# Optimization experiments

Measured on AMD Instinct MI355X. Metric: run time of the kernel, lower is better.

The kernel has to match this reference:

```python
import jax, jax.numpy as jnp
import numpy as np

D_MODEL, N_HEAD, N_KV_HEAD, D_HEAD = 1024, 16, 4, 64


def rotate_half(x):
    x1, x2 = x[..., : x.shape[-1] // 2], x[..., x.shape[-1] // 2:]
    return jnp.concatenate((-x2, x1), axis=-1)


def rope_cos_sin(seq_len, dim, dtype=jnp.float32):
    inv_freq = 1.0 / (10000.0 ** (jnp.arange(0, dim, 2, dtype=jnp.float32) / dim))
    t = jnp.arange(seq_len, dtype=jnp.float32)
    freqs = jnp.einsum('i,j->ij', t, inv_freq)          # [S, dim/2]
    emb = jnp.concatenate((freqs, freqs), axis=-1)       # [S, dim]
    return jnp.cos(emb).astype(dtype), jnp.sin(emb).astype(dtype)


def setup_inputs() -> dict:
    key = jax.random.key(0)
    ks = jax.random.split(key, 5)
    B, S = 2, 2048
    scale = 0.02
    return {
        'x': jax.random.normal(ks[0], (B, S, D_MODEL), dtype=jnp.float32),
        'Wq': jax.random.normal(ks[1], (D_MODEL, N_HEAD * D_HEAD), dtype=jnp.float32) * scale,
        'Wk': jax.random.normal(ks[2], (D_MODEL, N_KV_HEAD * D_HEAD), dtype=jnp.float32) * scale,
        'Wv': jax.random.normal(ks[3], (D_MODEL, N_KV_HEAD * D_HEAD), dtype=jnp.float32) * scale,
        'Wo': jax.random.normal(ks[4], (N_HEAD * D_HEAD, D_MODEL), dtype=jnp.float32) * scale,
    }


def reference(x, Wq, Wk, Wv, Wo):
    B, S, _ = x.shape
    scale = 1.0 / np.sqrt(D_HEAD)
    # projections -> [B, H, S, Dh]
    q = (x @ Wq).reshape(B, S, N_HEAD, D_HEAD).transpose(0, 2, 1, 3)
    k = (x @ Wk).reshape(B, S, N_KV_HEAD, D_HEAD).transpose(0, 2, 1, 3)
    v = (x @ Wv).reshape(B, S, N_KV_HEAD, D_HEAD).transpose(0, 2, 1, 3)
    cos, sin = rope_cos_sin(S, D_HEAD, x.dtype)          # [S, Dh]
    q = q * cos + rotate_half(q) * sin
    k = k * cos + rotate_half(k) * sin
    rep = N_HEAD // N_KV_HEAD
    k = jnp.repeat(k, rep, axis=1)                       # [B, H, S, Dh]
    v = jnp.repeat(v, rep, axis=1)
    scores = jnp.einsum('bhqd,bhkd->bhqk', q, k) * scale # [B, H, S, S]
    causal = jnp.triu(jnp.ones((S, S), dtype=bool), k=1)
    scores = jnp.where(causal, -jnp.inf, scores)
    probs = jax.nn.softmax(scores, axis=-1)
    ctx = jnp.einsum('bhqk,bhkd->bhqd', probs, v)        # [B, H, S, Dh]
    ctx = ctx.transpose(0, 2, 1, 3).reshape(B, S, N_HEAD * D_HEAD)
    return ctx @ Wo
```

## Files before the change

kernel.cpp:

```cpp
#include <hip/hip_runtime.h>
#include <hip/hip_bf16.h>
#include <cstdint>
#include <math.h>

#define S_LEN 2048
#define DM 1024
#define NQKV 1536
#define MROWS 4096
#define BKT 64

typedef __attribute__((ext_vector_type(8))) short short8;
typedef __attribute__((ext_vector_type(4))) float f32x4;
typedef __attribute__((ext_vector_type(16))) float f32x16;

#define QFOLD 0.18033688011112042f

__device__ __forceinline__ short f2bf(float x) {
  union { float f; uint32_t u; } v; v.f = x;
  uint32_t r = (v.u + 0x7fffu + ((v.u >> 16) & 1u)) >> 16;
  return (short)(uint16_t)r;
}

__device__ __forceinline__ uint32_t pk2(float a, float b) {
  __hip_bfloat162 h = __float22bfloat162_rn(make_float2(a, b));
  union { __hip_bfloat162 h2; uint32_t u; } cv; cv.h2 = h;
  return cv.u;
}

__global__ __launch_bounds__(256) void prep(const float* __restrict__ x,
    const float* __restrict__ Wq, const float* __restrict__ Wk,
    const float* __restrict__ Wv, const float* __restrict__ Wo,
    short* __restrict__ Xb, short* __restrict__ WcatT, short* __restrict__ WoT,
    float2* __restrict__ tab) {
  __shared__ short T[64 * 72];
  const int bb = blockIdx.x;
  const int tid = threadIdx.x;
  if (bb < 4096) {
    const int i = bb * 256 + tid;
    float4 v = ((const float4*)x)[i];
    short4 o;
    o.x = f2bf(v.x); o.y = f2bf(v.y); o.z = f2bf(v.z); o.w = f2bf(v.w);
    ((short4*)Xb)[i] = o;
    return;
  }
  if (bb >= 4736) {
    const int gid = (bb - 4736) * 256 + tid;
    #pragma unroll
    for (int e = 0; e < 4; ++e) {
      const int ii = gid + e * 16384;
      const int s = ii >> 5, j = ii & 31;
      const float inv = exp2f(-(float)j * 0.41524101186092029f);
      const float ang = (float)s * inv;
      tab[ii] = make_float2(cosf(ang), sinf(ang));
    }
    return;
  }
  const float* src; short* dst; int R, C, t2 = bb - 4096;
  if (t2 < 256)      { src = Wq; dst = WcatT;                        R = 1024; C = 1024; }
  else if (t2 < 320) { t2 -= 256; src = Wk; dst = WcatT + (size_t)1024*1024; R = 1024; C = 256; }
  else if (t2 < 384) { t2 -= 320; src = Wv; dst = WcatT + (size_t)1280*1024; R = 1024; C = 256; }
  else               { t2 -= 384; src = Wo; dst = WoT;               R = 1024; C = 1024; }
  const int r0 = (t2 & 15) * 64, c0 = (t2 >> 4) * 64;
  #pragma unroll
  for (int i = 0; i < 4; ++i) {
    int chunk = tid + i * 256;
    int r = chunk >> 4, cc = (chunk & 15) * 4;
    float4 v = *(const float4*)&src[(size_t)(r0 + r) * C + c0 + cc];
    T[(cc + 0) * 72 + r] = f2bf(v.x);
    T[(cc + 1) * 72 + r] = f2bf(v.y);
    T[(cc + 2) * 72 + r] = f2bf(v.z);
    T[(cc + 3) * 72 + r] = f2bf(v.w);
  }
  __syncthreads();
  #pragma unroll
  for (int i = 0; i < 2; ++i) {
    int chunk = tid + i * 256;
    int rr = chunk >> 3, kk = (chunk & 7) * 8;
    *(uint4*)&dst[(size_t)(c0 + rr) * R + r0 + kk] = *(uint4*)&T[rr * 72 + kk];
  }
}

template<int BMT, int BNT>
__global__ __launch_bounds__(256) void gemm_bf16_t(const short* __restrict__ A,
    const short* __restrict__ BT, float* __restrict__ C, int M, int N, int K) {
  constexpr int MI = BMT / 32, NI = BNT / 32;
  __shared__ short As[BMT * BKT];
  __shared__ short Bs[BNT * BKT];
  const int tid = threadIdx.x;
  const int wave = tid >> 6, lane = tid & 63;
  const int quad = lane >> 4, l15 = lane & 15;
  const int wm = (wave >> 1) * (BMT / 2), wn = (wave & 1) * (BNT / 2);
  const int m0 = blockIdx.y * BMT, n0 = blockIdx.x * BNT;
  const int rA = wave * (BMT / 4) + (lane >> 3);
  const int rB = wave * (BNT / 4) + (lane >> 3);
  const int scol = (lane & 7) * 8;

  f32x4 acc[MI][NI] = {};

  for (int k0 = 0; k0 < K; k0 += BKT) {
    __syncthreads();
    #pragma unroll
    for (int j = 0; j < MI; ++j)
      __builtin_amdgcn_global_load_lds(
          (const __attribute__((address_space(1))) void*)&A[(size_t)(m0 + rA + j * 8) * K + k0 + scol],
          (__attribute__((address_space(3))) void*)&As[(wave * MI + j) * 512],
          16, 0, 0);
    #pragma unroll
    for (int j = 0; j < NI; ++j)
      __builtin_amdgcn_global_load_lds(
          (const __attribute__((address_space(1))) void*)&BT[(size_t)(n0 + rB + j * 8) * K + k0 + scol],
          (__attribute__((address_space(3))) void*)&Bs[(wave * NI + j) * 512],
          16, 0, 0);
    __syncthreads();
    #pragma unroll
    for (int ks = 0; ks < 2; ++ks) {
      short8 af[MI], bfr[NI];
      #pragma unroll
      for (int mi = 0; mi < MI; ++mi)
        af[mi] = *(const short8*)&As[(wm + mi*16 + l15)*BKT + ks*32 + quad*8];
      #pragma unroll
      for (int ni = 0; ni < NI; ++ni)
        bfr[ni] = *(const short8*)&Bs[(wn + ni*16 + l15)*BKT + ks*32 + quad*8];
      #pragma unroll
      for (int mi = 0; mi < MI; ++mi)
        #pragma unroll
        for (int ni = 0; ni < NI; ++ni)
          acc[mi][ni] = __builtin_amdgcn_mfma_f32_16x16x32_bf16(af[mi], bfr[ni], acc[mi][ni], 0, 0, 0);
    }
  }
  #pragma unroll
  for (int mi = 0; mi < MI; ++mi)
    #pragma unroll
    for (int ni = 0; ni < NI; ++ni)
      #pragma unroll
      for (int r = 0; r < 4; ++r)
        C[(size_t)(m0 + wm + mi*16 + quad*4 + r)*N + (n0 + wn + ni*16 + l15)] = acc[mi][ni][r];
}

__global__ __launch_bounds__(256, 3) void gemm_qkv(const short* __restrict__ A,
    const short* __restrict__ BT, const float2* __restrict__ tab,
    short* __restrict__ Qb, short* __restrict__ Kb, short* __restrict__ Vt) {
  constexpr int MI = 2, NI = 4;
  __shared__ short SM[12288];
  short* As = SM;
  short* Bs = SM + 4096;
  const int tid = threadIdx.x;
  const int wave = tid >> 6, lane = tid & 63;
  const int quad = lane >> 4, l15 = lane & 15;
  const int wm = (wave >> 1) * 32, wn = (wave & 1) * 64;
  const int m0 = blockIdx.y * 64, n0 = blockIdx.x * 128;
  const int rA = wave * 16 + (lane >> 3);
  const int rB = wave * 32 + (lane >> 3);
  const int scol = (lane & 7) * 8;

  f32x4 acc[MI][NI] = {};

  for (int k0 = 0; k0 < DM; k0 += BKT) {
    __syncthreads();
    #pragma unroll
    for (int j = 0; j < MI; ++j)
      __builtin_amdgcn_global_load_lds(
          (const __attribute__((address_space(1))) void*)&A[(size_t)(m0 + rA + j * 8) * DM + k0 + scol],
          (__attribute__((address_space(3))) void*)&As[(wave * MI + j) * 512],
          16, 0, 0);
    #pragma unroll
    for (int j = 0; j < NI; ++j)
      __builtin_amdgcn_global_load_lds(
          (const __attribute__((address_space(1))) void*)&BT[(size_t)(n0 + rB + j * 8) * DM + k0 + scol],
          (__attribute__((address_space(3))) void*)&Bs[(wave * NI + j) * 512],
          16, 0, 0);
    __syncthreads();
    #pragma unroll
    for (int ks = 0; ks < 2; ++ks) {
      short8 af[MI], bfr[NI];
      #pragma unroll
      for (int mi = 0; mi < MI; ++mi)
        af[mi] = *(const short8*)&As[(wm + mi*16 + l15)*BKT + ks*32 + quad*8];
      #pragma unroll
      for (int ni = 0; ni < NI; ++ni)
        bfr[ni] = *(const short8*)&Bs[(wn + ni*16 + l15)*BKT + ks*32 + quad*8];
      #pragma unroll
      for (int mi = 0; mi < MI; ++mi)
        #pragma unroll
        for (int ni = 0; ni < NI; ++ni)
          acc[mi][ni] = __builtin_amdgcn_mfma_f32_16x16x32_bf16(af[mi], bfr[ni], acc[mi][ni], 0, 0, 0);
    }
  }

  const int c0 = n0 + wn;
  if (n0 < 1024) {
    #pragma unroll
    for (int mi = 0; mi < MI; ++mi)
      #pragma unroll
      for (int r = 0; r < 4; ++r) {
        const int row = m0 + wm + mi*16 + quad*4 + r;
        const int s = row & (S_LEN - 1);
        #pragma unroll
        for (int ni = 0; ni < 2; ++ni) {
          const int j = ni*16 + l15;
          const float2 cn = tab[s*32 + j];
          const float x1 = acc[mi][ni][r], x2 = acc[mi][ni+2][r];
          Qb[(size_t)row*1024 + c0 + j]      = f2bf((x1*cn.x - x2*cn.y) * QFOLD);
          Qb[(size_t)row*1024 + c0 + j + 32] = f2bf((x2*cn.x + x1*cn.y) * QFOLD);
        }
      }
  } else if (n0 < 1280) {
    const int hh = (c0 - 1024) >> 6;
    #pragma unroll
    for (int mi = 0; mi < MI; ++mi)
      #pragma unroll
      for (int r = 0; r < 4; ++r) {
        const int row = m0 + wm + mi*16 + quad*4 + r;
        const int s = row & (S_LEN - 1);
        const int sw = (s & 7) << 3;
        #pragma unroll
        for (int ni = 0; ni < 2; ++ni) {
          const int j = ni*16 + l15;
          const float2 cn = tab[s*32 + j];
          const float x1 = acc[mi][ni][r], x2 = acc[mi][ni+2][r];
          Kb[(size_t)row*256 + hh*64 + (j ^ sw)]        = f2bf(x1*cn.x - x2*cn.y);
          Kb[(size_t)row*256 + hh*64 + ((j + 32) ^ sw)] = f2bf(x2*cn.x + x1*cn.y);
        }
      }
  } else {
    __syncthreads();
    #pragma unroll
    for (int mi = 0; mi < MI; ++mi)
      #pragma unroll
      for (int ni = 0; ni < NI; ++ni) {
        short4 p;
        p.x = f2bf(acc[mi][ni][0]); p.y = f2bf(acc[mi][ni][1]);
        p.z = f2bf(acc[mi][ni][2]); p.w = f2bf(acc[mi][ni][3]);
        *(short4*)&SM[(wn + ni*16 + l15)*80 + wm + mi*16 + quad*4] = p;
      }
    __syncthreads();
    const int b_ = m0 >> 11, sbase = m0 & (S_LEN - 1);
    #pragma unroll
    for (int i = 0; i < 4; ++i) {
      const int chunk = tid + i * 256;
      const int vl = chunk >> 3;
      const int kk = (chunk & 7) * 8;
      const int vcol = (n0 - 1280) + vl;
      const int kvh = vcol >> 6, dd = vcol & 63;
      uint4 v = *(uint4*)&SM[vl*80 + kk];
      *(uint4*)&Vt[((size_t)((b_*4 + kvh)*64 + dd))*S_LEN + sbase + (kk ^ ((dd & 7) << 3))] = v;
    }
  }
}

__global__ __launch_bounds__(256, 3) void fattn13(const short* __restrict__ Qb,
    const short* __restrict__ Kb, const short* __restrict__ Vt, short* __restrict__ Ctx) {
  __shared__ short SMEM[24576];
  const int idx = blockIdx.x;
  const int kk_ = (idx & 255) >> 3;
  const int jt  = (idx >> 8) ? kk_ : 63 - kk_;
  const int b   = (idx >> 2) & 1;
  const int kvh = idx & 3;
  const int tid = threadIdx.x, wav = tid >> 6, lane = tid & 63;
  const int l31 = lane & 31, hi = lane >> 5;
  const int h = kvh * 4 + wav;
  const int sx = (l31 & 7) << 3;
  const size_t qbase  = (size_t)b * S_LEN * 1024;
  const size_t kbase  = (size_t)b * S_LEN * 256;
  const size_t vtbase = (size_t)(b * 4 + kvh) * 64 * S_LEN;

  const short* kptr = Kb + kbase + (size_t)(tid >> 3) * 256 + kvh * 64 + (tid & 7) * 8;
  const short* vptr = Vt + vtbase + (size_t)(tid >> 3) * 2048 + (tid & 7) * 8;

#define STAGE(u) do { \
    const int bi_ = (u) % 3; \
    const short* kp_ = kptr + (size_t)(u) * 16384; \
    const short* vp_ = vptr + (u) * 64; \
    short* kd_ = &SMEM[bi_ * 8192 + tid * 8]; \
    short* vd_ = &SMEM[bi_ * 8192 + 4096 + tid * 8]; \
    _Pragma("unroll") \
    for (int i_ = 0; i_ < 2; ++i_) { \
      __builtin_amdgcn_global_load_lds((const __attribute__((address_space(1))) void*)(kp_ + i_ * 8192), \
          (__attribute__((address_space(3))) void*)(kd_ + i_ * 2048), 16, 0, 0); \
      __builtin_amdgcn_global_load_lds((const __attribute__((address_space(1))) void*)(vp_ + i_ * 65536), \
          (__attribute__((address_space(3))) void*)(vd_ + i_ * 2048), 16, 0, 0); \
    } \
  } while (0)

  const int q0 = jt * 32;
  const int ntiles = (jt >> 1) + 1;
  const int qg = q0 + l31;

  short8 qf[4];
  {
    const short* qp = &Qb[qbase + (size_t)qg * 1024 + h * 64 + hi * 8];
    #pragma unroll
    for (int ks = 0; ks < 4; ++ks) qf[ks] = *(const short8*)(qp + ks * 16);
  }

  f32x16 O0 = {}, O1 = {};
  float la0 = 0.f, la1 = 0.f, la2 = 0.f, la3 = 0.f;

  STAGE(0);
  if (ntiles > 1) STAGE(1);

  for (int t = 0; t < ntiles; ++t) {
    const int k0 = t * 64;
    const int rem = ntiles - 1 - t;
    if (rem >= 1) { asm volatile("s_waitcnt vmcnt(4)" ::: "memory"); }
    else          { asm volatile("s_waitcnt vmcnt(0)" ::: "memory"); }
    __builtin_amdgcn_sched_barrier(0);
    __builtin_amdgcn_s_barrier();
    if (t + 2 < ntiles) STAGE(t + 2);

    const short* ks_ = &SMEM[(t % 3) * 8192];
    const short* vs_ = &SMEM[(t % 3) * 8192 + 4096];

    f32x16 sc[2];
    __builtin_amdgcn_s_setprio(1);
    #pragma unroll
    for (int kt = 0; kt < 2; ++kt) {
      const int r = kt * 32 + l31;
      f32x16 a = {};
      #pragma unroll
      for (int ks2 = 0; ks2 < 4; ++ks2) {
        short8 kf = *(const short8*)&ks_[r * 64 + ((ks2 * 16 + hi * 8) ^ sx)];
        a = __builtin_amdgcn_mfma_f32_32x32x16_bf16(kf, qf[ks2], a, 0, 0, 0);
      }
      sc[kt] = a;
    }
    __builtin_amdgcn_s_setprio(0);

    if (t == ntiles - 1) {
      #pragma unroll
      for (int kt = 0; kt < 2; ++kt)
        #pragma unroll
        for (int r = 0; r < 16; ++r) {
          const int kvg = k0 + kt * 32 + (r & 3) + 8 * (r >> 2) + 4 * hi;
          if (kvg > qg) sc[kt][r] = -1e30f;
        }
    }

    short8 af[4];
    #pragma unroll
    for (int kt = 0; kt < 2; ++kt) {
      #pragma unroll
      for (int r = 0; r < 16; ++r) sc[kt][r] = exp2f(sc[kt][r]);
      la0 += (sc[kt][0] + sc[kt][1]) + (sc[kt][2] + sc[kt][3]);
      la1 += (sc[kt][4] + sc[kt][5]) + (sc[kt][6] + sc[kt][7]);
      la2 += (sc[kt][8] + sc[kt][9]) + (sc[kt][10] + sc[kt][11]);
      la3 += (sc[kt][12] + sc[kt][13]) + (sc[kt][14] + sc[kt][15]);
      #pragma unroll
      for (int st = 0; st < 2; ++st) {
        uint32_t x0 = pk2(sc[kt][st * 8 + 0], sc[kt][st * 8 + 1]);
        uint32_t x1 = pk2(sc[kt][st * 8 + 2], sc[kt][st * 8 + 3]);
        uint32_t x2 = pk2(sc[kt][st * 8 + 4], sc[kt][st * 8 + 5]);
        uint32_t x3 = pk2(sc[kt][st * 8 + 6], sc[kt][st * 8 + 7]);
        asm("v_permlane32_swap_b32 %0, %1" : "+v"(x0), "+v"(x2));
        asm("v_permlane32_swap_b32 %0, %1" : "+v"(x1), "+v"(x3));
        union { short8 s8; uint32_t u[4]; } cv;
        cv.u[0] = x0; cv.u[1] = x1; cv.u[2] = x2; cv.u[3] = x3;
        af[kt * 2 + st] = cv.s8;
      }
    }

    __builtin_amdgcn_s_setprio(1);
    #pragma unroll
    for (int s = 0; s < 4; ++s) {
      const int co = s * 16 + hi * 8;
      short8 bv0 = *(const short8*)&vs_[l31 * 64 + (co ^ sx)];
      O0 = __builtin_amdgcn_mfma_f32_32x32x16_bf16(af[s], bv0, O0, 0, 0, 0);
      short8 bv1 = *(const short8*)&vs_[(32 + l31) * 64 + (co ^ sx)];
      O1 = __builtin_amdgcn_mfma_f32_32x32x16_bf16(af[s], bv1, O1, 0, 0, 0);
    }
    __builtin_amdgcn_s_setprio(0);
  }

  float ll = (la0 + la1) + (la2 + la3);
  ll += __shfl_xor(ll, 32, 64);
  const float inv = 1.0f / ll;
  #pragma unroll
  for (int r = 0; r < 16; ++r) {
    const int crow = (r & 3) + 8 * (r >> 2) + 4 * hi;
    const float invr = __shfl(inv, crow, 64);
    const size_t o = qbase + (size_t)(q0 + crow) * 1024 + h * 64;
    Ctx[o + l31]      = f2bf(O0[r] * invr);
    Ctx[o + 32 + l31] = f2bf(O1[r] * invr);
  }
#undef STAGE
}

extern "C" void kernel_launch(void* const* d_in, const int* in_sizes, int n_in,
                              void* d_out, int out_size, void* d_ws, size_t ws_size,
                              hipStream_t stream) {
  const float* x  = (const float*)d_in[0];
  const float* Wq = (const float*)d_in[1];
  const float* Wk = (const float*)d_in[2];
  const float* Wv = (const float*)d_in[3];
  const float* Wo = (const float*)d_in[4];
  float* out = (float*)d_out;

  char* w = (char*)d_ws;
  short*  Xb    = (short*)w;   w += (size_t)MROWS * DM * 2;
  short*  WcatT = (short*)w;   w += (size_t)NQKV * DM * 2;
  short*  WoT   = (short*)w;   w += (size_t)DM * DM * 2;
  short*  Qbuf  = (short*)w;   w += (size_t)MROWS * DM * 2;
  short*  Kbuf  = (short*)w;   w += (size_t)MROWS * 256 * 2;
  short*  Vt    = (short*)w;   w += (size_t)8 * 64 * S_LEN * 2;
  short*  Ctx   = (short*)w;   w += (size_t)MROWS * DM * 2;
  float2* tab   = (float2*)w;  w += (size_t)S_LEN * 32 * 8;

  prep<<<dim3(4800), dim3(256), 0, stream>>>(x, Wq, Wk, Wv, Wo, Xb, WcatT, WoT, tab);

  gemm_qkv<<<dim3(NQKV / 128, MROWS / 64), dim3(256), 0, stream>>>(Xb, WcatT, tab, Qbuf, Kbuf, Vt);
  fattn13<<<dim3(512), dim3(256), 0, stream>>>(Qbuf, Kbuf, Vt, Ctx);
  gemm_bf16_t<64,128><<<dim3(DM / 128, MROWS / 64), dim3(256), 0, stream>>>(Ctx, WoT, out, MROWS, DM, DM);
}
```

Measured before the change: 167.5 us.

## Double-buffer LDS tiles in QKV and output GEMMs to overlap loads with MFMA

```diff
diff --git a/kernel.cpp b/kernel.cpp
--- a/kernel.cpp
+++ b/kernel.cpp
@@ -81,11 +81,12 @@
 }
 
 template<int BMT, int BNT>
-__global__ __launch_bounds__(256) void gemm_bf16_t(const short* __restrict__ A,
+__global__ __launch_bounds__(256, 3) void gemm_bf16_t(const short* __restrict__ A,
     const short* __restrict__ BT, float* __restrict__ C, int M, int N, int K) {
   constexpr int MI = BMT / 32, NI = BNT / 32;
-  __shared__ short As[BMT * BKT];
-  __shared__ short Bs[BNT * BKT];
+  static_assert(MI + NI == 6, "vmcnt literal assumes 6 loads/thread/step");
+  __shared__ short As[2 * BMT * BKT];
+  __shared__ short Bs[2 * BNT * BKT];
   const int tid = threadIdx.x;
   const int wave = tid >> 6, lane = tid & 63;
   const int quad = lane >> 4, l15 = lane & 15;
@@ -97,30 +98,46 @@
 
   f32x4 acc[MI][NI] = {};
 
-  for (int k0 = 0; k0 < K; k0 += BKT) {
-    __syncthreads();
-    #pragma unroll
-    for (int j = 0; j < MI; ++j)
-      __builtin_amdgcn_global_load_lds(
-          (const __attribute__((address_space(1))) void*)&A[(size_t)(m0 + rA + j * 8) * K + k0 + scol],
-          (__attribute__((address_space(3))) void*)&As[(wave * MI + j) * 512],
-          16, 0, 0);
-    #pragma unroll
-    for (int j = 0; j < NI; ++j)
-      __builtin_amdgcn_global_load_lds(
-          (const __attribute__((address_space(1))) void*)&BT[(size_t)(n0 + rB + j * 8) * K + k0 + scol],
-          (__attribute__((address_space(3))) void*)&Bs[(wave * NI + j) * 512],
-          16, 0, 0);
-    __syncthreads();
+#define GSTAGE(u) do { \
+    const int bi_ = (u) & 1; const int k0_ = (u) * BKT; \
+    _Pragma("unroll") \
+    for (int j = 0; j < MI; ++j) \
+      __builtin_amdgcn_global_load_lds( \
+          (const __attribute__((address_space(1))) void*)&A[(size_t)(m0 + rA + j * 8) * K + k0_ + scol], \
+          (__attribute__((address_space(3))) void*)&As[bi_ * BMT * BKT + (wave * MI + j) * 512], 16, 0, 0); \
+    _Pragma("unroll") \
+    for (int j = 0; j < NI; ++j) \
+      __builtin_amdgcn_global_load_lds( \
+          (const __attribute__((address_space(1))) void*)&BT[(size_t)(n0 + rB + j * 8) * K + k0_ + scol], \
+          (__attribute__((address_space(3))) void*)&Bs[bi_ * BNT * BKT + (wave * NI + j) * 512], 16, 0, 0); \
+  } while (0)
+
+  const int nk = K / BKT;
+  GSTAGE(0);
+  for (int t = 0; t < nk; ++t) {
+    __builtin_amdgcn_sched_barrier(0);
+    __builtin_amdgcn_s_barrier();
+    __builtin_amdgcn_sched_barrier(0);
+    if (t + 1 < nk) {
+      GSTAGE(t + 1);
+      asm volatile("s_waitcnt vmcnt(6)" ::: "memory");
+    } else {
+      asm volatile("s_waitcnt vmcnt(0)" ::: "memory");
+    }
+    __builtin_amdgcn_sched_barrier(0);
+    __builtin_amdgcn_s_barrier();
+    __builtin_amdgcn_sched_barrier(0);
+    const short* As_ = &As[(t & 1) * BMT * BKT];
+    const short* Bs_ = &Bs[(t & 1) * BNT * BKT];
     #pragma unroll
     for (int ks = 0; ks < 2; ++ks) {
       short8 af[MI], bfr[NI];
       #pragma unroll
       for (int mi = 0; mi < MI; ++mi)
-        af[mi] = *(const short8*)&As[(wm + mi*16 + l15)*BKT + ks*32 + quad*8];
+        af[mi] = *(const short8*)&As_[(wm + mi*16 + l15)*BKT + ks*32 + quad*8];
       #pragma unroll
       for (int ni = 0; ni < NI; ++ni)
-        bfr[ni] = *(const short8*)&Bs[(wn + ni*16 + l15)*BKT + ks*32 + quad*8];
+        bfr[ni] = *(const short8*)&Bs_[(wn + ni*16 + l15)*BKT + ks*32 + quad*8];
       #pragma unroll
       for (int mi = 0; mi < MI; ++mi)
         #pragma unroll
@@ -128,6 +145,7 @@
           acc[mi][ni] = __builtin_amdgcn_mfma_f32_16x16x32_bf16(af[mi], bfr[ni], acc[mi][ni], 0, 0, 0);
     }
   }
+#undef GSTAGE
   #pragma unroll
   for (int mi = 0; mi < MI; ++mi)
     #pragma unroll
@@ -141,9 +159,9 @@
     const short* __restrict__ BT, const float2* __restrict__ tab,
     short* __restrict__ Qb, short* __restrict__ Kb, short* __restrict__ Vt) {
   constexpr int MI = 2, NI = 4;
-  __shared__ short SM[12288];
+  __shared__ short SM[24576];
   short* As = SM;
-  short* Bs = SM + 4096;
+  short* Bs = SM + 8192;
   const int tid = threadIdx.x;
   const int wave = tid >> 6, lane = tid & 63;
   const int quad = lane >> 4, l15 = lane & 15;
@@ -155,30 +173,46 @@
 
   f32x4 acc[MI][NI] = {};
 
-  for (int k0 = 0; k0 < DM; k0 += BKT) {
-    __syncthreads();
-    #pragma unroll
-    for (int j = 0; j < MI; ++j)
-      __builtin_amdgcn_global_load_lds(
-          (const __attribute__((address_space(1))) void*)&A[(size_t)(m0 + rA + j * 8) * DM + k0 + scol],
-          (__attribute__((address_space(3))) void*)&As[(wave * MI + j) * 512],
-          16, 0, 0);
-    #pragma unroll
-    for (int j = 0; j < NI; ++j)
-      __builtin_amdgcn_global_load_lds(
-          (const __attribute__((address_space(1))) void*)&BT[(size_t)(n0 + rB + j * 8) * DM + k0 + scol],
-          (__attribute__((address_space(3))) void*)&Bs[(wave * NI + j) * 512],
-          16, 0, 0);
-    __syncthreads();
+#define QSTAGE(u) do { \
+    const int bi_ = (u) & 1; const int k0_ = (u) * BKT; \
+    _Pragma("unroll") \
+    for (int j = 0; j < MI; ++j) \
+      __builtin_amdgcn_global_load_lds( \
+          (const __attribute__((address_space(1))) void*)&A[(size_t)(m0 + rA + j * 8) * DM + k0_ + scol], \
+          (__attribute__((address_space(3))) void*)&As[bi_ * 4096 + (wave * MI + j) * 512], 16, 0, 0); \
+    _Pragma("unroll") \
+    for (int j = 0; j < NI; ++j) \
+      __builtin_amdgcn_global_load_lds( \
+          (const __attribute__((address_space(1))) void*)&BT[(size_t)(n0 + rB + j * 8) * DM + k0_ + scol], \
+          (__attribute__((address_space(3))) void*)&Bs[bi_ * 8192 + (wave * NI + j) * 512], 16, 0, 0); \
+  } while (0)
+
+  const int nk = DM / BKT;
+  QSTAGE(0);
+  for (int t = 0; t < nk; ++t) {
+    __builtin_amdgcn_sched_barrier(0);
+    __builtin_amdgcn_s_barrier();
+    __builtin_amdgcn_sched_barrier(0);
+    if (t + 1 < nk) {
+      QSTAGE(t + 1);
+      asm volatile("s_waitcnt vmcnt(6)" ::: "memory");
+    } else {
+      asm volatile("s_waitcnt vmcnt(0)" ::: "memory");
+    }
+    __builtin_amdgcn_sched_barrier(0);
+    __builtin_amdgcn_s_barrier();
+    __builtin_amdgcn_sched_barrier(0);
+    const short* As_ = &As[(t & 1) * 4096];
+    const short* Bs_ = &Bs[(t & 1) * 8192];
     #pragma unroll
     for (int ks = 0; ks < 2; ++ks) {
       short8 af[MI], bfr[NI];
       #pragma unroll
       for (int mi = 0; mi < MI; ++mi)
-        af[mi] = *(const short8*)&As[(wm + mi*16 + l15)*BKT + ks*32 + quad*8];
+        af[mi] = *(const short8*)&As_[(wm + mi*16 + l15)*BKT + ks*32 + quad*8];
       #pragma unroll
       for (int ni = 0; ni < NI; ++ni)
-        bfr[ni] = *(const short8*)&Bs[(wn + ni*16 + l15)*BKT + ks*32 + quad*8];
+        bfr[ni] = *(const short8*)&Bs_[(wn + ni*16 + l15)*BKT + ks*32 + quad*8];
       #pragma unroll
       for (int mi = 0; mi < MI; ++mi)
         #pragma unroll
@@ -186,6 +220,7 @@
           acc[mi][ni] = __builtin_amdgcn_mfma_f32_16x16x32_bf16(af[mi], bfr[ni], acc[mi][ni], 0, 0, 0);
     }
   }
+#undef QSTAGE
 
   const int c0 = n0 + wn;
   if (n0 < 1024) {
```

Result: no change. 166.8 us (-0.4%).
